# Kernel tuning notes

Hardware: AMD Instinct MI355X
Metric: run time of the kernel (lower is better)

The kernel has to match this reference:

```python
import jax, jax.numpy as jnp
import numpy as np

TAU = 2.0      # spikingjelly LIFNode tau
V_TH = 1.0     # default v_threshold
ALPHA = 2.0    # default ATan surrogate alpha
T_STEPS = 32   # output_size (repeat count along time)

# Heaviside spike with ATan surrogate gradient (spikingjelly surrogate.ATan)
@jax.custom_vjp
def spike_fn(x):
    return (x >= 0.0).astype(x.dtype)

def _spike_fwd(x):
    return spike_fn(x), x

def _spike_bwd(x, g):
    sg = (ALPHA / 2.0) / (1.0 + (jnp.pi / 2.0 * ALPHA * x) ** 2)
    return (g * sg,)

spike_fn.defvjp(_spike_fwd, _spike_bwd)


def setup_inputs() -> dict:
    key = jax.random.key(0)
    inputs = jax.random.normal(key, (64, 64, 512), dtype=jnp.float32)  # [B, C, L]
    return {"inputs": inputs}


def reference(inputs):
    # repeat([T,1,1,1]) then permute(0,1,3,2): every step sees the same [B,L,C] frame
    xt = jnp.transpose(inputs, (0, 2, 1))  # [B, L, C]
    v0 = jnp.zeros_like(xt)                # v_reset = 0.0 initial membrane

    def step(v, _):
        # LIF with decay_input=True, hard reset to v_reset=0:
        # v = v + (x - (v - v_reset)) / tau
        v = v + (xt - v) / TAU
        s = spike_fn(v - V_TH)
        # hard reset; detach_reset=True -> spike detached in reset path
        v = v * (1.0 - jax.lax.stop_gradient(s))
        return v, s

    _, spks = jax.lax.scan(step, v0, None, length=T_STEPS)  # [T, B, L, C]
    return jnp.transpose(spks, (1, 0, 2, 3))                # [B, T, L, C]
```

## Files before the change

kernel.cpp:

```cpp
#include <hip/hip_runtime.h>


constexpr int B = 64;
constexpr int C = 64;
constexpr int L = 512;
constexpr int T = 32;

typedef float vf4 __attribute__((ext_vector_type(4)));

__global__ __launch_bounds__(256) void lif_repeat_kernel(
    const float* __restrict__ in, float* __restrict__ out) {
  __shared__ float lds[16 * 64];
  const int blk = blockIdx.x;
  const int tid = threadIdx.x;
  const int b  = blk >> 5;
  const int l0 = (blk & 31) * 16;

  {
    const int c = tid >> 2;
    const int q = tid & 3;
    const vf4 v = *(const vf4*)(in + (size_t)b * (C * L) + (size_t)c * L + l0 + q * 4);
    float* p = lds + c;
    p[(q * 4 + 0) * 64] = v.x;
    p[(q * 4 + 1) * 64] = v.y;
    p[(q * 4 + 2) * 64] = v.z;
    p[(q * 4 + 3) * 64] = v.w;
  }
  __syncthreads();

  const int c4 = tid & 15;
  const int ll = tid >> 4;
  const vf4 x = *(const vf4*)(lds + ll * 64 + c4 * 4);

  vf4* op = (vf4*)(out + (size_t)b * (T * L * C) + (size_t)(l0 + ll) * C + c4 * 4);
  constexpr int t_stride4 = (L * C) / 4;

  float v0 = 0.f, v1 = 0.f, v2 = 0.f, v3 = 0.f;
#pragma unroll
  for (int t = 0; t < T; ++t) {
    v0 += (x.x - v0) * 0.5f;
    v1 += (x.y - v1) * 0.5f;
    v2 += (x.z - v2) * 0.5f;
    v3 += (x.w - v3) * 0.5f;
    vf4 s;
    s.x = (v0 >= 1.0f) ? 1.0f : 0.0f;
    s.y = (v1 >= 1.0f) ? 1.0f : 0.0f;
    s.z = (v2 >= 1.0f) ? 1.0f : 0.0f;
    s.w = (v3 >= 1.0f) ? 1.0f : 0.0f;
    __builtin_nontemporal_store(s, op + (size_t)t * t_stride4);
    v0 = (s.x != 0.0f) ? 0.0f : v0;
    v1 = (s.y != 0.0f) ? 0.0f : v1;
    v2 = (s.z != 0.0f) ? 0.0f : v2;
    v3 = (s.w != 0.0f) ? 0.0f : v3;
  }
}

extern "C" void kernel_launch(void* const* d_in, const int* in_sizes, int n_in,
                              void* d_out, int out_size, void* d_ws, size_t ws_size,
                              hipStream_t stream) {
  const float* in = (const float*)d_in[0];
  float* out = (float*)d_out;
  const int grid = B * 32;
  lif_repeat_kernel<<<grid, 256, 0, stream>>>(in, out);
}
```

Measured before the change: 272.5 us.

## Process 64 L-positions per block with 4 rows per thread and regular stores

Each block now covers 64 sequence positions instead of 16, and each thread runs the LIF recurrence for four rows. The grid shrinks fourfold to 512 blocks. The nontemporal output stores become plain stores, and the time loop is only partly unrolled. The aim is to amortise block launch and the LDS transpose over more output and to keep more stores in flight per thread, at the cost of fewer blocks for the GPU's many CUs and different cache behaviour for the 268MB write stream.

After: 259.3 us. 4.8% less time.

```diff
diff --git a/kernel.cpp b/kernel.cpp
--- a/kernel.cpp
+++ b/kernel.cpp
@@ -10,48 +10,60 @@
 
 __global__ __launch_bounds__(256) void lif_repeat_kernel(
     const float* __restrict__ in, float* __restrict__ out) {
-  __shared__ float lds[16 * 64];
-  const int blk = blockIdx.x;
+  __shared__ float lds[64 * 64];
   const int tid = threadIdx.x;
-  const int b  = blk >> 5;
-  const int l0 = (blk & 31) * 16;
+  const int b  = blockIdx.x >> 3;
+  const int l0 = (blockIdx.x & 7) * 64;
 
   {
     const int c = tid >> 2;
     const int q = tid & 3;
-    const vf4 v = *(const vf4*)(in + (size_t)b * (C * L) + (size_t)c * L + l0 + q * 4);
-    float* p = lds + c;
-    p[(q * 4 + 0) * 64] = v.x;
-    p[(q * 4 + 1) * 64] = v.y;
-    p[(q * 4 + 2) * 64] = v.z;
-    p[(q * 4 + 3) * 64] = v.w;
+    const float* ip = in + (size_t)b * (C * L) + (size_t)c * L + l0;
+#pragma unroll
+    for (int k = 0; k < 4; ++k) {
+      const int lo = q * 4 + k * 16;
+      const vf4 v = *(const vf4*)(ip + lo);
+      lds[(lo + 0) * 64 + c] = v.x;
+      lds[(lo + 1) * 64 + c] = v.y;
+      lds[(lo + 2) * 64 + c] = v.z;
+      lds[(lo + 3) * 64 + c] = v.w;
+    }
   }
   __syncthreads();
 
   const int c4 = tid & 15;
-  const int ll = tid >> 4;
-  const vf4 x = *(const vf4*)(lds + ll * 64 + c4 * 4);
+  const int rr = tid >> 4;
+  float x[4][4], v[4][4];
+#pragma unroll
+  for (int j = 0; j < 4; ++j) {
+    const vf4 xv = *(const vf4*)(lds + (rr + 16 * j) * 64 + c4 * 4);
+    x[j][0] = xv.x; x[j][1] = xv.y; x[j][2] = xv.z; x[j][3] = xv.w;
+    v[j][0] = v[j][1] = v[j][2] = v[j][3] = 0.f;
+  }
 
-  vf4* op = (vf4*)(out + (size_t)b * (T * L * C) + (size_t)(l0 + ll) * C + c4 * 4);
-  constexpr int t_stride4 = (L * C) / 4;
+  float* const obase = out + (size_t)b * (T * L * C) + (size_t)l0 * C + c4 * 4;
+  constexpr size_t t_stride = (size_t)L * C;
 
-  float v0 = 0.f, v1 = 0.f, v2 = 0.f, v3 = 0.f;
+#pragma unroll 2
+  for (int t = 0; t < T; ++t) {
+    float* ot = obase + (size_t)t * t_stride;
 #pragma unroll
-  for (int t = 0; t < T; ++t) {
-    v0 += (x.x - v0) * 0.5f;
-    v1 += (x.y - v1) * 0.5f;
-    v2 += (x.z - v2) * 0.5f;
-    v3 += (x.w - v3) * 0.5f;
-    vf4 s;
-    s.x = (v0 >= 1.0f) ? 1.0f : 0.0f;
-    s.y = (v1 >= 1.0f) ? 1.0f : 0.0f;
-    s.z = (v2 >= 1.0f) ? 1.0f : 0.0f;
-    s.w = (v3 >= 1.0f) ? 1.0f : 0.0f;
-    __builtin_nontemporal_store(s, op + (size_t)t * t_stride4);
-    v0 = (s.x != 0.0f) ? 0.0f : v0;
-    v1 = (s.y != 0.0f) ? 0.0f : v1;
-    v2 = (s.z != 0.0f) ? 0.0f : v2;
-    v3 = (s.w != 0.0f) ? 0.0f : v3;
+    for (int j = 0; j < 4; ++j) {
+      vf4 s;
+#pragma unroll
+      for (int i = 0; i < 4; ++i) {
+        v[j][i] += (x[j][i] - v[j][i]) * 0.5f;
+      }
+      s.x = (v[j][0] >= 1.0f) ? 1.0f : 0.0f;
+      s.y = (v[j][1] >= 1.0f) ? 1.0f : 0.0f;
+      s.z = (v[j][2] >= 1.0f) ? 1.0f : 0.0f;
+      s.w = (v[j][3] >= 1.0f) ? 1.0f : 0.0f;
+      *(vf4*)(ot + (size_t)(rr + 16 * j) * C) = s;
+#pragma unroll
+      for (int i = 0; i < 4; ++i) {
+        v[j][i] = (v[j][i] >= 1.0f) ? 0.0f : v[j][i];
+      }
+    }
   }
 }
 
@@ -60,6 +72,6 @@
                               hipStream_t stream) {
   const float* in = (const float*)d_in[0];
   float* out = (float*)d_out;
-  const int grid = B * 32;
+  const int grid = B * (L / 64);
   lif_repeat_kernel<<<grid, 256, 0, stream>>>(in, out);
 }
```
